# Optimization experiments

Measured on AMD Instinct MI355X. Metric: run time of the kernel, lower is better.

Reference implementation:

```python
import jax, jax.numpy as jnp
import numpy as np

H = 512; EMB = 300; TAGE = 20; TRE = 20
VOCAB = 50000; NTAGS = 50; NTRANS = 100; NCONST = 80
B = 128; S = 256; T = 512; R = S // 2


def _lstm_scan(x, Wih, Whh, b):
    # x: [N, L, D] -> hidden states [N, L, H]; torch gate order i, f, g, o
    N = x.shape[0]; Hh = Whh.shape[1]
    xg = jnp.einsum('nld,gd->nlg', x, Wih) + b  # precompute input projections
    def step(carry, xg_t):
        h, c = carry
        g = xg_t + h @ Whh.T
        i, f, gg, o = jnp.split(g, 4, axis=-1)
        c = jax.nn.sigmoid(f) * c + jax.nn.sigmoid(i) * jnp.tanh(gg)
        h = jax.nn.sigmoid(o) * jnp.tanh(c)
        return (h, c), h
    h0 = jnp.zeros((N, Hh), x.dtype)
    _, hs = jax.lax.scan(step, (h0, h0), jnp.swapaxes(xg, 0, 1))
    return jnp.swapaxes(hs, 0, 1)


def setup_inputs() -> dict:
    key = jax.random.key(0)
    ks = iter(jax.random.split(key, 40))
    def p(shape, scale):
        return jax.random.normal(next(ks), shape, jnp.float32) * jnp.float32(scale)
    def lstm_p(din):
        s = 1.0 / np.sqrt(H)
        return p((4 * H, din), s), p((4 * H, H), s), p((4 * H,), s)
    inp = {}
    inp['word_idx'] = jax.random.randint(next(ks), (B, S), 0, VOCAB)
    inp['tag_idx'] = jax.random.randint(next(ks), (B, S), 0, NTAGS)
    inp['transition_idx'] = jax.random.randint(next(ks), (B, T), 0, NTRANS)
    inp['label_idx'] = jax.random.randint(next(ks), (B, R), 0, NCONST)
    inp['emb'] = p((VOCAB, EMB), 1.0)
    inp['tag_emb'] = p((NTAGS, TAGE), 1.0)
    inp['tr_emb'] = p((NTRANS, TRE), 1.0)
    inp['const_emb'] = p((NCONST, H), 1.0)
    inp['word_Wih'], inp['word_Whh'], inp['word_b'] = lstm_p(EMB + TAGE)
    inp['tr_Wih'], inp['tr_Whh'], inp['tr_b'] = lstm_p(TRE)
    inp['con_Wih'], inp['con_Whh'], inp['con_b'] = lstm_p(H)
    inp['fwd_Wih'], inp['fwd_Whh'], inp['fwd_b'] = lstm_p(H)
    inp['bwd_Wih'], inp['bwd_Whh'], inp['bwd_b'] = lstm_p(H)
    inp['w2c_W'] = p((H, H), 1.0 / np.sqrt(H)); inp['w2c_b'] = jnp.zeros((H,), jnp.float32)
    inp['red_W'] = p((H, 2 * H), 1.0 / np.sqrt(2 * H)); inp['red_b'] = jnp.zeros((H,), jnp.float32)
    inp['out_W'] = p((NTRANS, 3 * H), 1.0 / np.sqrt(3 * H)); inp['out_b'] = jnp.zeros((NTRANS,), jnp.float32)
    return inp


def reference(word_idx, tag_idx, transition_idx, label_idx, emb, tag_emb, tr_emb, const_emb, word_Wih, word_Whh, word_b, tr_Wih, tr_Whh, tr_b, con_Wih, con_Whh, con_b, fwd_Wih, fwd_Whh, fwd_b, bwd_Wih, bwd_Whh, bwd_b, w2c_W, w2c_b, red_W, red_b, out_W, out_b):
    Bn, Sn = word_idx.shape
    Rn = label_idx.shape[1]
    # initial_word_queue: word emb + tag emb -> word LSTM
    word_in = jnp.concatenate([emb[word_idx], tag_emb[tag_idx]], axis=-1)  # [B,S,EMB+TAGE]
    word_h = _lstm_scan(word_in, word_Wih, word_Whh, word_b)              # [B,S,H]
    # transform_word_to_constituent
    c0 = word_h @ w2c_W.T + w2c_b                                         # [B,S,H]
    # build_constituent: label emb + 2 children through fwd/bwd reduce LSTMs
    lab = const_emb[label_idx]                                            # [B,R,H]
    ch0 = c0[:, 0::2][:, :Rn]; ch1 = c0[:, 1::2][:, :Rn]
    fwd_seq = jnp.stack([lab, ch0, ch1], axis=2).reshape(Bn * Rn, 3, -1)
    bwd_seq = jnp.stack([lab, ch1, ch0], axis=2).reshape(Bn * Rn, 3, -1)
    fh = _lstm_scan(fwd_seq, fwd_Wih, fwd_Whh, fwd_b)[:, -1]
    bh = _lstm_scan(bwd_seq, bwd_Wih, bwd_Whh, bwd_b)[:, -1]
    red = jnp.tanh(jnp.concatenate([fh, bh], -1) @ red_W.T + red_b).reshape(Bn, Rn, -1)
    # push_constituent: constituent LSTMCell scan over built constituents
    const_h = _lstm_scan(red, con_Wih, con_Whh, con_b)[:, -1]             # [B,H]
    # push_transition: transition LSTMCell scan
    tr_h = _lstm_scan(tr_emb[transition_idx], tr_Wih, tr_Whh, tr_b)[:, -1]  # [B,H]
    # forward(): W over concat(word_hx, transition_hx, constituent_hx)
    hx = jnp.concatenate([word_h[:, -1], tr_h, const_h], axis=-1)         # [B,3H]
    return hx @ out_W.T + out_b                                           # [B,NTRANS]
```

## Files before the change

### kernel.cpp

```cpp
#include <hip/hip_runtime.h>

typedef unsigned short u16;
typedef unsigned int u32;
typedef unsigned long long u64;
typedef __attribute__((ext_vector_type(8))) short short8;
typedef __attribute__((ext_vector_type(4))) float f32x4;
typedef __attribute__((ext_vector_type(4))) unsigned int u32x4;

namespace {
constexpr int kS  = 256;
constexpr int kT  = 512;
constexpr int kNT = 100;
constexpr int LDST = 40;
constexpr u32 POISON = 0xFFFFFFFFu;
}

__device__ __forceinline__ float bf(u16 v){ return __uint_as_float(((u32)v)<<16); }
__device__ __forceinline__ u16 f2bf(float f){
  u32 u = __float_as_uint(f);
  return (u16)((u + 0x7fffu + ((u>>16)&1u)) >> 16);
}
__device__ __forceinline__ float sigm(float x){ return 1.f/(1.f+__expf(-x)); }
__device__ __forceinline__ float tanha(float x){ return 2.f/(1.f+__expf(-2.f*x)) - 1.f; }
__device__ __forceinline__ float wred(float v){
  #pragma unroll
  for (int off=32; off>0; off>>=1) v += __shfl_xor(v, off, 64);
  return v;
}
__device__ __forceinline__ short8 as_s8(u32x4 x){ union{u32x4 q; short8 v;} u; u.q=x; return u.v; }
__device__ __forceinline__ u32 chk4(u32x4 v){
  return (u32)((v.x==POISON)|(v.y==POISON)|(v.z==POISON)|(v.w==POISON));
}

#define LDX(d, b, o) asm volatile("global_load_dwordx4 %0, %1, off offset:" o : "=v"(d) : "v"(b))
#define LDP(d, b, o) asm volatile("global_load_dwordx4 %0, %1, off offset:" o " sc0 sc1" : "=v"(d) : "v"(b))
#define LDI(d, b)    asm volatile("global_load_dword %0, %1, off" : "=v"(d) : "v"(b))
#define STW(p, v)    asm volatile("global_store_dword %0, %1, off sc0 sc1" :: "v"(p), "v"(v) : "memory")
#define WAITV0       do{ asm volatile("s_waitcnt vmcnt(0)" ::: "memory"); __builtin_amdgcn_sched_barrier(0); }while(0)

__global__ void k_fill(u32* __restrict__ p, int n4){
  const int i = blockIdx.x*256 + threadIdx.x;
  if (i < n4) {
    u32x4 v = {POISON, POISON, POISON, POISON};
    *(u32x4*)&p[(size_t)i*4] = v;
  }
}

struct SeqJob {
  u16* hseq;
  const u16* xg; const int* idx;
  float* c_io;
  const u16* Bw;
  int s_begin, s_end, mode, smask, c_store;
};

__global__ __launch_bounds__(256,1) void k_seq2(SeqJob jA, SeqJob jB)
{
  __shared__ u16 Bs[32*520];
  __shared__ float c_lds[128*9];
  __shared__ float sc[4*4*16*20];
  const SeqJob j = (blockIdx.x < 64) ? jA : jB;
  const int gb = blockIdx.x & 63;
  const int tid = threadIdx.x;
  const int ln = tid & 63, w = tid >> 6, wm = w * 32;
  const int fr = ln & 15, koff = (ln >> 4) * 8;
  const int n0 = gb * 32, jh0 = gb * 8;

  for (int e = tid; e < 2048; e += 256) {
    const int cl_ = e >> 6, kb = (e & 63) * 8;
    *(u32x4*)&Bs[cl_*520 + kb] = *(const u32x4*)&j.Bw[(size_t)(n0+cl_)*512 + kb];
  }
  for (int e = tid; e < 1024; e += 256) {
    const int m = e >> 3, jj = e & 7;
    c_lds[m*9 + jj] = j.c_io[(size_t)m*512 + jh0 + jj];
  }
  __syncthreads();

  const size_t aoff0 = (size_t)(wm + fr)*512 + koff;
  const size_t aoff1 = (size_t)(wm + 16 + fr)*512 + koff;
  const int cr = (ln>>4)*4, cc = ln&15;
  const int trow = ln>>2, pp = ln&3, ntp = pp>>1, cp = pp&1;
  const f32x4 z4 = {0.f,0.f,0.f,0.f};
  const int mA = wm + trow;
  const int mB = wm + 16 + trow;
  const int xgcol = n0 + ntp*16 + cp*8;

  u32x4 xqA, xqB;
  {
    long ivA = mA, ivB = mB;
    if (j.mode == 1) {
      ivA = j.idx[(size_t)mA*512 + j.s_begin];
      ivB = j.idx[(size_t)mB*512 + j.s_begin];
    } else if (j.mode == 2) {
      ivA = (long)mA*128 + j.s_begin;
      ivB = (long)mB*128 + j.s_begin;
    }
    const u16* xgs0 = (j.mode == 0) ? (j.xg + (size_t)j.s_begin*262144) : j.xg;
    const u16* pA = &xgs0[(size_t)ivA*2048 + xgcol];
    const u16* pB = &xgs0[(size_t)ivB*2048 + xgcol];
    LDX(xqA, pA, "0");
    LDX(xqB, pB, "0");
  }
  int inA = 0, inB = 0;

#define PISS(kt, o) LDP(aq0[kt], pa0, o); LDP(aq1[kt], pa1, o)
#define ISSUE_ALL \
  PISS(0,"0");    PISS(1,"64");   PISS(2,"128");  PISS(3,"192"); \
  PISS(4,"256");  PISS(5,"320");  PISS(6,"384");  PISS(7,"448"); \
  PISS(8,"512");  PISS(9,"576");  PISS(10,"640"); PISS(11,"704"); \
  PISS(12,"768"); PISS(13,"832"); PISS(14,"896"); PISS(15,"960")
#define CHECK_ALL(bad) \
  { bad = 0; _Pragma("unroll") \
    for (int kt = 0; kt < 16; ++kt) bad |= chk4(aq0[kt]) | chk4(aq1[kt]); }

  for (int s = j.s_begin; s < j.s_end; ++s) {
    const u16* Ab = j.hseq + (size_t)((s-1) & j.smask)*65536;
    u16* hout     = j.hseq + (size_t)(s & j.smask)*65536;
    const u16* pa0 = Ab + aoff0;
    const u16* pa1 = Ab + aoff1;
    const bool more = (s + 1 < j.s_end);

    if (j.mode == 1 && more) {
      const int* ia = &j.idx[(size_t)mA*512 + s + 1];
      const int* ib = &j.idx[(size_t)mB*512 + s + 1];
      LDI(inA, ia);
      LDI(inB, ib);
    }

    u32x4 aq0[16], aq1[16];
    ISSUE_ALL;
    WAITV0;
    u32 bad; CHECK_ALL(bad);
    while (bad) {
      __builtin_amdgcn_s_sleep(1);
      ISSUE_ALL;
      WAITV0;
      CHECK_ALL(bad);
    }

    f32x4 acc[2][2] = {{z4,z4},{z4,z4}};
    #pragma unroll
    for (int kt = 0; kt < 16; ++kt) {
      const short8 b0 = *(const short8*)&Bs[fr*520 + kt*32 + koff];
      const short8 b1 = *(const short8*)&Bs[(16+fr)*520 + kt*32 + koff];
      const short8 a0v = as_s8(aq0[kt]);
      const short8 a1v = as_s8(aq1[kt]);
      acc[0][0] = __builtin_amdgcn_mfma_f32_16x16x32_bf16(a0v, b0, acc[0][0], 0,0,0);
      acc[0][1] = __builtin_amdgcn_mfma_f32_16x16x32_bf16(a0v, b1, acc[0][1], 0,0,0);
      acc[1][0] = __builtin_amdgcn_mfma_f32_16x16x32_bf16(a1v, b0, acc[1][0], 0,0,0);
      acc[1][1] = __builtin_amdgcn_mfma_f32_16x16x32_bf16(a1v, b1, acc[1][1], 0,0,0);
    }

    #pragma unroll
    for (int mt=0; mt<2; ++mt)
      #pragma unroll
      for (int nt=0; nt<2; ++nt) {
        float* scb = &sc[(size_t)(w*4 + mt*2 + nt)*320];
        #pragma unroll
        for (int ri=0; ri<4; ++ri) scb[(cr+ri)*20 + cc] = acc[mt][nt][ri];
      }
    #pragma unroll
    for (int mt=0; mt<2; ++mt) {
      const int m = mt ? mB : mA;
      const float* scb = &sc[(size_t)(w*4+mt*2+ntp)*320 + trow*20 + cp*8];
      const float4 zlo = *(const float4*)&scb[0];
      const float4 zhi = *(const float4*)&scb[4];
      union { u32x4 u4; u16 h[8]; } xq;
      xq.u4 = mt ? xqB : xqA;
      const int cj = m*9 + ntp*4 + cp*2;
      float h0, h1;
      {
        const float i_ = sigm(zlo.x + bf(xq.h[0]));
        const float f_ = sigm(zlo.y + bf(xq.h[1]));
        const float g_ = tanha(zlo.z + bf(xq.h[2]));
        const float o_ = sigm(zlo.w + bf(xq.h[3]));
        const float cn = f_*c_lds[cj] + i_*g_;
        c_lds[cj] = cn;
        h0 = o_*tanha(cn);
      }
      {
        const float i_ = sigm(zhi.x + bf(xq.h[4]));
        const float f_ = sigm(zhi.y + bf(xq.h[5]));
        const float g_ = tanha(zhi.z + bf(xq.h[6]));
        const float o_ = sigm(zhi.w + bf(xq.h[7]));
        const float cn = f_*c_lds[cj+1] + i_*g_;
        c_lds[cj+1] = cn;
        h1 = o_*tanha(cn);
      }
      const u32 pk = (u32)f2bf(h0) | ((u32)f2bf(h1) << 16);
      u32* hp = (u32*)&hout[(size_t)m*512 + jh0 + ntp*4 + cp*2];
      STW(hp, pk);
    }

    if (more) {
      const u16* xgs1 = (j.mode == 0) ? (j.xg + (size_t)(s+1)*262144) : j.xg;
      long xrA = (j.mode == 0) ? (long)mA : (j.mode == 1 ? (long)inA : ((long)mA*128 + s + 1));
      long xrB = (j.mode == 0) ? (long)mB : (j.mode == 1 ? (long)inB : ((long)mB*128 + s + 1));
      const u16* pA = &xgs1[(size_t)xrA*2048 + xgcol];
      const u16* pB = &xgs1[(size_t)xrB*2048 + xgcol];
      LDX(xqA, pA, "0");
      LDX(xqB, pB, "0");
    }
  }
  if (j.c_store) {
    __syncthreads();
    for (int e = tid; e < 1024; e += 256) {
      const int m = e >> 3, jj = e & 7;
      j.c_io[(size_t)m*512 + jh0 + jj] = c_lds[m*9 + jj];
    }
  }
#undef PISS
#undef ISSUE_ALL
#undef CHECK_ALL
}

__device__ __forceinline__ void gemm_core(
    const u16* __restrict__ A, const u16* __restrict__ B, int K,
    int m0, int n0, u16* As, u16* Bs, f32x4 acc[4][4], int tid)
{
  const int lane = tid & 63;
  const int w = tid >> 6;
  const int wm = (w & 1) * 64, wn = (w >> 1) * 64;
  const int fr = lane & 15;
  const int fq = (lane >> 4) * 8;
  for (int k0 = 0; k0 < K; k0 += 32) {
    __syncthreads();
    #pragma unroll
    for (int it = 0; it < 2; ++it) {
      const int l = tid + it * 256;
      const int r = l >> 2, kq = (l & 3) * 8;
      *(uint4*)&As[r * LDST + kq] = *(const uint4*)&A[(size_t)(m0 + r) * K + k0 + kq];
      *(uint4*)&Bs[r * LDST + kq] = *(const uint4*)&B[(size_t)(n0 + r) * K + k0 + kq];
    }
    __syncthreads();
    short8 af[4], bfr[4];
    #pragma unroll
    for (int t = 0; t < 4; ++t) {
      af[t]  = *(const short8*)&As[(wm + t * 16 + fr) * LDST + fq];
      bfr[t] = *(const short8*)&Bs[(wn + t * 16 + fr) * LDST + fq];
    }
    #pragma unroll
    for (int mt = 0; mt < 4; ++mt)
      #pragma unroll
      for (int nt = 0; nt < 4; ++nt)
        acc[mt][nt] = __builtin_amdgcn_mfma_f32_16x16x32_bf16(af[mt], bfr[nt], acc[mt][nt], 0, 0, 0);
  }
}

__global__ __launch_bounds__(256) void k_gemm(
    const u16* __restrict__ A, const u16* __restrict__ B, u16* __restrict__ C,
    const float* __restrict__ bias, int K, int N, int tanh_flag)
{
  __shared__ u16 As[128 * LDST];
  __shared__ u16 Bs[128 * LDST];
  const int tid = threadIdx.x;
  const int m0 = blockIdx.x * 128, n0 = blockIdx.y * 128;
  f32x4 acc[4][4];
  const f32x4 z4 = {0.f, 0.f, 0.f, 0.f};
  #pragma unroll
  for (int mt = 0; mt < 4; ++mt)
    #pragma unroll
    for (int nt = 0; nt < 4; ++nt) acc[mt][nt] = z4;

  gemm_core(A, B, K, m0, n0, As, Bs, acc, tid);

  const int lane = tid & 63;
  const int w = tid >> 6;
  const int wm = (w & 1) * 64, wn = (w >> 1) * 64;
  const int cr = (lane >> 4) * 4, cc = lane & 15;
  #pragma unroll
  for (int mt = 0; mt < 4; ++mt)
    #pragma unroll
    for (int nt = 0; nt < 4; ++nt)
      #pragma unroll
      for (int ri = 0; ri < 4; ++ri) {
        const int row = m0 + wm + mt * 16 + cr + ri;
        const int col = n0 + wn + nt * 16 + cc;
        float v = acc[mt][nt][ri];
        if (bias) v += bias[col];
        if (tanh_flag) v = tanha(v);
        C[(size_t)row * N + col] = f2bf(v);
      }
}

__global__ __launch_bounds__(256) void k_lstm_cat(
    const u16* __restrict__ H, const u16* __restrict__ X,
    const u16* __restrict__ B, const float* __restrict__ bias,
    const int* __restrict__ idx, int cmode, int p0, int first,
    float* __restrict__ c_st, u16* __restrict__ h_out, int h_stride, int h_coloff)
{
  __shared__ u16 As[128 * LDST];
  __shared__ u16 Bs[128 * LDST];
  __shared__ float zb[64 * 128];
  const int tid = threadIdx.x;
  const int m0 = blockIdx.x * 128, n0 = blockIdx.y * 128;
  const int lane = tid & 63;
  const int w = tid >> 6;
  const int wm = (w & 1) * 64, wn = (w >> 1) * 64;
  const int fr = lane & 15, fq = (lane >> 4) * 8;
  f32x4 acc[4][4];
  const f32x4 z4 = {0.f, 0.f, 0.f, 0.f};
  #pragma unroll
  for (int mt = 0; mt < 4; ++mt)
    #pragma unroll
    for (int nt = 0; nt < 4; ++nt) acc[mt][nt] = z4;

  for (int k0 = first ? 512 : 0; k0 < 1024; k0 += 32) {
    __syncthreads();
    #pragma unroll
    for (int it = 0; it < 2; ++it) {
      const int l = tid + it * 256;
      const int r = l >> 2, kq = (l & 3) * 8;
      const int m = m0 + r;
      const u16* src;
      if (k0 < 512) {
        src = H + (size_t)m * 512 + k0 + kq;
      } else {
        long xr;
        if (cmode == 1)      xr = (long)(2 * (m & 127) + p0) * 128 + (m >> 7);
        else if (cmode == 2) xr = (long)idx[m];
        else                 xr = (long)m * 128 + p0;
        src = X + (size_t)xr * 512 + (k0 - 512) + kq;
      }
      *(uint4*)&As[r * LDST + kq] = *(const uint4*)src;
      *(uint4*)&Bs[r * LDST + kq] = *(const uint4*)&B[(size_t)(n0 + r) * 1024 + k0 + kq];
    }
    __syncthreads();
    short8 af[4], bfr[4];
    #pragma unroll
    for (int t = 0; t < 4; ++t) {
      af[t]  = *(const short8*)&As[(wm + t * 16 + fr) * LDST + fq];
      bfr[t] = *(const short8*)&Bs[(wn + t * 16 + fr) * LDST + fq];
    }
    #pragma unroll
    for (int mt = 0; mt < 4; ++mt)
      #pragma unroll
      for (int nt = 0; nt < 4; ++nt)
        acc[mt][nt] = __builtin_amdgcn_mfma_f32_16x16x32_bf16(af[mt], bfr[nt], acc[mt][nt], 0, 0, 0);
  }

  const int cr = (lane >> 4) * 4, cc = lane & 15;
  #pragma unroll
  for (int half = 0; half < 2; ++half) {
    __syncthreads();
    if (wm == half * 64) {
      #pragma unroll
      for (int mt = 0; mt < 4; ++mt)
        #pragma unroll
        for (int nt = 0; nt < 4; ++nt)
          #pragma unroll
          for (int ri = 0; ri < 4; ++ri)
            zb[(mt * 16 + cr + ri) * 128 + wn + nt * 16 + cc] = acc[mt][nt][ri];
    }
    __syncthreads();
    for (int c = tid; c < 2048; c += 256) {
      const int rl = c >> 5;
      const int q  = c & 31;
      const int m  = m0 + half * 64 + rl;
      const int jh = (n0 >> 2) + q;
      const float4 bv = *(const float4*)&bias[n0 + q * 4];
      const float4 zv = *(const float4*)&zb[rl * 128 + q * 4];
      const float i_ = sigm(zv.x + bv.x);
      const float f_ = sigm(zv.y + bv.y);
      const float g_ = tanha(zv.z + bv.z);
      const float o_ = sigm(zv.w + bv.w);
      const size_t ci = (size_t)m * 512 + jh;
      const float cold = first ? 0.f : c_st[ci];
      const float cn = f_ * cold + i_ * g_;
      c_st[ci] = cn;
      h_out[(size_t)m * h_stride + h_coloff + jh] = f2bf(o_ * tanha(cn));
    }
  }
}

__global__ __launch_bounds__(256) void k_gate0(
    const u16* __restrict__ xg, int xg_mode, int p0,
    const int* __restrict__ idx, int istride,
    float* __restrict__ c_st, u16* __restrict__ h_out, int h_stride, int h_coloff, int M)
{
  const int id = blockIdx.x * 256 + threadIdx.x;
  if (id >= M * 512) return;
  const int m = id >> 9, jh = id & 511;
  long xr;
  if (xg_mode == 0) xr = (long)m * p0;
  else              xr = (long)idx[(size_t)m * istride];
  const ushort4 xq = *(const ushort4*)&xg[(size_t)xr * 2048 + jh * 4];
  const float i_ = sigm(bf(xq.x));
  const float g_ = tanha(bf(xq.z));
  const float o_ = sigm(bf(xq.w));
  const float cn = i_ * g_;
  c_st[(size_t)m * 512 + jh] = cn;
  h_out[(size_t)m * h_stride + h_coloff + jh] = f2bf(o_ * tanha(cn));
}

__global__ void k_perm_w(const float* __restrict__ in, u16* __restrict__ out,
                         int Ksrc, int Kfill, int Ktot, int coff)
{
  const int rp = blockIdx.x;
  const int g = rp & 3, jh = rp >> 2;
  const float* src = in + (size_t)(g * 512 + jh) * Ksrc;
  for (int k = threadIdx.x; k < Kfill; k += 256)
    out[(size_t)rp * Ktot + coff + k] = f2bf(k < Ksrc ? src[k] : 0.f);
}
__global__ void k_perm_b(const float* __restrict__ in, float* __restrict__ out)
{
  const int rp = blockIdx.x * 256 + threadIdx.x;
  out[rp] = in[(rp & 3) * 512 + (rp >> 2)];
}
__global__ void k_cvt(const float* __restrict__ in, u16* __restrict__ out, int n)
{
  const int i = blockIdx.x * 256 + threadIdx.x;
  if (i < n) out[i] = f2bf(in[i]);
}
__global__ void k_pad2d(const float* __restrict__ in, u16* __restrict__ out,
                        int Rin, int Kin, int Kout)
{
  const int r = blockIdx.x;
  for (int k = threadIdx.x; k < Kout; k += 256)
    out[(size_t)r * Kout + k] = f2bf((r < Rin && k < Kin) ? in[(size_t)r * Kin + k] : 0.f);
}
__global__ void k_gather_word(const int* __restrict__ widx, const int* __restrict__ tidx,
                              const float* __restrict__ emb, const float* __restrict__ temb,
                              u16* __restrict__ Aw)
{
  const int row = blockIdx.x;
  const int s = row >> 7, b = row & 127;
  const int wi = widx[b * kS + s];
  const int ti = tidx[b * kS + s];
  for (int t = threadIdx.x; t < 320; t += 256)
    Aw[(size_t)row * 320 + t] = f2bf(t < 300 ? emb[(size_t)wi * 300 + t] : temb[ti * 20 + t - 300]);
}

__global__ __launch_bounds__(256) void k_out(
    const u16* __restrict__ wh, const u16* __restrict__ trh, const u16* __restrict__ conh,
    const float* __restrict__ W, const float* __restrict__ bias, float* __restrict__ out)
{
  const int wid = blockIdx.x * 4 + (threadIdx.x >> 6);
  const int lane = threadIdx.x & 63;
  const int b = wid / kNT;
  const int t = wid - b * kNT;
  const u16* s0 = wh + (size_t)b * 512;
  const u16* s1 = trh + (size_t)b * 512;
  const u16* s2 = conh + (size_t)b * 512;
  const float* wr = W + (size_t)t * 1536;
  float acc = 0.f;
  #pragma unroll
  for (int i = 0; i < 8; ++i) acc += bf(s0[i * 64 + lane]) * wr[i * 64 + lane];
  #pragma unroll
  for (int i = 0; i < 8; ++i) acc += bf(s1[i * 64 + lane]) * wr[512 + i * 64 + lane];
  #pragma unroll
  for (int i = 0; i < 8; ++i) acc += bf(s2[i * 64 + lane]) * wr[1024 + i * 64 + lane];
  acc = wred(acc);
  if (lane == 0) out[(size_t)b * kNT + t] = acc + bias[t];
}

extern "C" void kernel_launch(void* const* d_in, const int* in_sizes, int n_in,
                              void* d_out, int out_size, void* d_ws, size_t ws_size,
                              hipStream_t stream)
{
  (void)in_sizes; (void)n_in; (void)out_size; (void)ws_size;
  const int* word_idx = (const int*)d_in[0];
  const int* tag_idx  = (const int*)d_in[1];
  const int* tr_idx   = (const int*)d_in[2];
  const int* lab_idx  = (const int*)d_in[3];
  const float* emb       = (const float*)d_in[4];
  const float* tag_emb   = (const float*)d_in[5];
  const float* tr_emb    = (const float*)d_in[6];
  const float* const_emb = (const float*)d_in[7];
  const float* word_Wih = (const float*)d_in[8];
  const float* word_Whh = (const float*)d_in[9];
  const float* word_b   = (const float*)d_in[10];
  const float* tr_Wih = (const float*)d_in[11];
  const float* tr_Whh = (const float*)d_in[12];
  const float* tr_b   = (const float*)d_in[13];
  const float* con_Wih = (const float*)d_in[14];
  const float* con_Whh = (const float*)d_in[15];
  const float* con_b   = (const float*)d_in[16];
  const float* fwd_Wih = (const float*)d_in[17];
  const float* fwd_Whh = (const float*)d_in[18];
  const float* fwd_b   = (const float*)d_in[19];
  const float* bwd_Wih = (const float*)d_in[20];
  const float* bwd_Whh = (const float*)d_in[21];
  const float* bwd_b   = (const float*)d_in[22];
  const float* w2c_W = (const float*)d_in[23];
  const float* w2c_b = (const float*)d_in[24];
  const float* red_W = (const float*)d_in[25];
  const float* red_b = (const float*)d_in[26];
  const float* out_W = (const float*)d_in[27];
  const float* out_b = (const float*)d_in[28];

  char* p = (char*)d_ws;
  auto alloc = [&](size_t bytes)->void* {
    void* r = (void*)p; p += (bytes + 255) & ~(size_t)255; return r;
  };
  u16* word_h = (u16*)alloc((size_t)33554432);
  char* R     = (char*)alloc((size_t)167772160);
  u16* A_word = (u16*)(R);
  u16* XGword = (u16*)(R + 33554432);
  u16* trseq  = (u16*)(R);
  u16* c0     = (u16*)(R + 33554432);
  u16* h1     = (u16*)(R + 67108864);
  u16* h2     = (u16*)(R + 83886080);
  float* c_big= (float*)(R + 100663296);
  u16* fb     = (u16*)(R + 134217728);
  u16* red    = (u16*)(R);
  u16* XG_con = (u16*)(R + 67108864);
  u16* conseq = (u16*)(R + 134217728);
  u16* wWih = (u16*)alloc((size_t)2048*320*2);
  u16* wWhh = (u16*)alloc((size_t)2048*512*2);
  u16* tWih = (u16*)alloc((size_t)2048*32*2);
  u16* tWhh = (u16*)alloc((size_t)2048*512*2);
  u16* cWihp = (u16*)alloc((size_t)2048*512*2);
  u16* cWhhp = (u16*)alloc((size_t)2048*512*2);
  u16* fWcat = (u16*)alloc((size_t)2048*1024*2);
  u16* bWcat = (u16*)alloc((size_t)2048*1024*2);
  u16* fWih  = (u16*)alloc((size_t)2048*512*2);
  u16* bWih  = (u16*)alloc((size_t)2048*512*2);
  u16* w2cWb = (u16*)alloc((size_t)512*512*2);
  u16* redWb = (u16*)alloc((size_t)512*1024*2);
  u16* A80   = (u16*)alloc((size_t)128*512*2);
  u16* Atr   = (u16*)alloc((size_t)128*32*2);
  u16* tbltr = (u16*)alloc((size_t)128*2048*2);
  u16* tbl0  = (u16*)alloc((size_t)128*2048*2);
  float* b_word = (float*)alloc(2048*4);
  float* b_tr   = (float*)alloc(2048*4);
  float* b_con  = (float*)alloc(2048*4);
  float* b_fwd  = (float*)alloc(2048*4);
  float* b_bwd  = (float*)alloc(2048*4);
  float* c_word = (float*)alloc((size_t)128*512*4);
  float* c_tr   = (float*)alloc((size_t)128*512*4);
  float* c_con  = (float*)alloc((size_t)128*512*4);

  k_perm_w<<<2048,256,0,stream>>>(word_Wih, wWih, 320, 320, 320, 0);
  k_perm_w<<<2048,256,0,stream>>>(word_Whh, wWhh, 512, 512, 512, 0);
  k_perm_w<<<2048,256,0,stream>>>(tr_Wih,   tWih, 20,  32,  32,  0);
  k_perm_w<<<2048,256,0,stream>>>(tr_Whh,   tWhh, 512, 512, 512, 0);
  k_perm_w<<<2048,256,0,stream>>>(con_Wih,  cWihp, 512, 512, 512, 0);
  k_perm_w<<<2048,256,0,stream>>>(con_Whh,  cWhhp, 512, 512, 512, 0);
  k_perm_w<<<2048,256,0,stream>>>(fwd_Whh,  fWcat, 512, 512, 1024, 0);
  k_perm_w<<<2048,256,0,stream>>>(fwd_Wih,  fWcat, 512, 512, 1024, 512);
  k_perm_w<<<2048,256,0,stream>>>(bwd_Whh,  bWcat, 512, 512, 1024, 0);
  k_perm_w<<<2048,256,0,stream>>>(bwd_Wih,  bWcat, 512, 512, 1024, 512);
  k_perm_w<<<2048,256,0,stream>>>(fwd_Wih,  fWih, 512, 512, 512, 0);
  k_perm_w<<<2048,256,0,stream>>>(bwd_Wih,  bWih, 512, 512, 512, 0);
  k_perm_b<<<8,256,0,stream>>>(word_b, b_word);
  k_perm_b<<<8,256,0,stream>>>(tr_b,   b_tr);
  k_perm_b<<<8,256,0,stream>>>(con_b,  b_con);
  k_perm_b<<<8,256,0,stream>>>(fwd_b,  b_fwd);
  k_perm_b<<<8,256,0,stream>>>(bwd_b,  b_bwd);
  k_cvt<<<1024,256,0,stream>>>(w2c_W, w2cWb, 512*512);
  k_cvt<<<2048,256,0,stream>>>(red_W, redWb, 512*1024);
  k_pad2d<<<128,256,0,stream>>>(const_emb, A80, 80, 512, 512);
  k_pad2d<<<128,256,0,stream>>>(tr_emb,    Atr, 100, 20, 32);
  k_gather_word<<<32768,256,0,stream>>>(word_idx, tag_idx, emb, tag_emb, A_word);

  k_gemm<<<dim3(256,16),256,0,stream>>>(A_word, wWih, XGword, b_word, 320, 2048, 0);
  k_gemm<<<dim3(1,16),256,0,stream>>>(Atr, tWih, tbltr, b_tr, 32, 2048, 0);

  k_fill<<<8160,256,0,stream>>>((u32*)(word_h + 65536), 2088960);
  k_fill<<<8160,256,0,stream>>>((u32*)(trseq + 65536), 2088960);

  k_gate0<<<256,256,0,stream>>>(XGword, 0, 1, nullptr, 0, c_word, word_h, 512, 0, 128);
  k_gate0<<<256,256,0,stream>>>(tbltr, 2, 0, tr_idx, 512, c_tr, trseq, 512, 0, 128);

  SeqJob jw { word_h, XGword, nullptr, c_word, wWhh, 1, 256, 0, 255, 0 };
  SeqJob jt1{ trseq,  tbltr,  tr_idx,  c_tr,   tWhh, 1, 256, 1, 511, 1 };
  k_seq2<<<128,256,0,stream>>>(jw, jt1);

  k_gemm<<<dim3(256,4),256,0,stream>>>(word_h, w2cWb, c0, w2c_b, 512, 512, 0);

  k_gemm<<<dim3(1,16),256,0,stream>>>(A80, fWih, tbl0, b_fwd, 512, 2048, 0);
  k_gate0<<<32768,256,0,stream>>>(tbl0, 2, 0, lab_idx, 1, c_big, h1, 512, 0, 16384);
  k_lstm_cat<<<dim3(128,16),256,0,stream>>>(h1, c0, fWcat, b_fwd, nullptr, 1, 0, 0, c_big, h2, 512, 0);
  k_lstm_cat<<<dim3(128,16),256,0,stream>>>(h2, c0, fWcat, b_fwd, nullptr, 1, 1, 0, c_big, fb, 1024, 0);
  k_gemm<<<dim3(1,16),256,0,stream>>>(A80, bWih, tbl0, b_bwd, 512, 2048, 0);
  k_gate0<<<32768,256,0,stream>>>(tbl0, 2, 0, lab_idx, 1, c_big, h1, 512, 0, 16384);
  k_lstm_cat<<<dim3(128,16),256,0,stream>>>(h1, c0, bWcat, b_bwd, nullptr, 1, 1, 0, c_big, h2, 512, 0);
  k_lstm_cat<<<dim3(128,16),256,0,stream>>>(h2, c0, bWcat, b_bwd, nullptr, 1, 0, 0, c_big, fb, 1024, 512);

  k_gemm<<<dim3(128,4),256,0,stream>>>(fb, redWb, red, red_b, 1024, 512, 1);

  k_gemm<<<dim3(128,16),256,0,stream>>>(red, cWihp, XG_con, b_con, 512, 2048, 0);

  k_fill<<<8192,256,0,stream>>>((u32*)(trseq + (size_t)256*65536), 2097152);
  k_fill<<<4064,256,0,stream>>>((u32*)(conseq + 65536), 1040384);

  k_gate0<<<256,256,0,stream>>>(XG_con, 0, 128, nullptr, 0, c_con, conseq, 512, 0, 128);

  SeqJob jc { conseq, XG_con, nullptr, c_con, cWhhp, 1,   128, 2, 255, 0 };
  SeqJob jt2{ trseq,  tbltr,  tr_idx,  c_tr,  tWhh,  256, 512, 1, 511, 0 };
  k_seq2<<<128,256,0,stream>>>(jc, jt2);

  k_out<<<3200,256,0,stream>>>(word_h + (size_t)255*65536, trseq + (size_t)511*65536,
                               conseq + (size_t)127*65536, out_W, out_b, (float*)d_out);
}
```

Measured before the change: 6.373 ms.

## Replace poison-polling recurrence sync with per-step flags and XCD-local block placement

The persistent LSTM recurrence kernel stops spinning on poison-filled hidden-state buffers and instead uses per-block step flags, published after a block barrier and polled by one wavefront. The kernel now launches 512 blocks and discovers which blocks share an XCD by probing L2 visibility. When one group of 64 co-located blocks is verified, it runs a job using L2-scoped (sc0) loads and stores instead of system-coherent ones. This also removes the poison fill kernels. The cost is a complex startup handshake and extra idle blocks, with a fallback to the old placement and system-scope traffic if discovery fails. It also relies on undocumented XCD scheduling behaviour.

```diff
diff --git a/kernel.cpp b/kernel.cpp
--- a/kernel.cpp
+++ b/kernel.cpp
@@ -12,7 +12,6 @@
 constexpr int kT  = 512;
 constexpr int kNT = 100;
 constexpr int LDST = 40;
-constexpr u32 POISON = 0xFFFFFFFFu;
 }
 
 __device__ __forceinline__ float bf(u16 v){ return __uint_as_float(((u32)v)<<16); }
@@ -28,22 +27,41 @@
   return v;
 }
 __device__ __forceinline__ short8 as_s8(u32x4 x){ union{u32x4 q; short8 v;} u; u.q=x; return u.v; }
-__device__ __forceinline__ u32 chk4(u32x4 v){
-  return (u32)((v.x==POISON)|(v.y==POISON)|(v.z==POISON)|(v.w==POISON));
-}
-
-#define LDX(d, b, o) asm volatile("global_load_dwordx4 %0, %1, off offset:" o : "=v"(d) : "v"(b))
-#define LDP(d, b, o) asm volatile("global_load_dwordx4 %0, %1, off offset:" o " sc0 sc1" : "=v"(d) : "v"(b))
-#define LDI(d, b)    asm volatile("global_load_dword %0, %1, off" : "=v"(d) : "v"(b))
-#define STW(p, v)    asm volatile("global_store_dword %0, %1, off sc0 sc1" :: "v"(p), "v"(v) : "memory")
-#define WAITV0       do{ asm volatile("s_waitcnt vmcnt(0)" ::: "memory"); __builtin_amdgcn_sched_barrier(0); }while(0)
-
-__global__ void k_fill(u32* __restrict__ p, int n4){
+
+__device__ __forceinline__ void st_sys_u32(u32* p, u32 v){
+  __hip_atomic_store(p, v, __ATOMIC_RELAXED, __HIP_MEMORY_SCOPE_SYSTEM);
+}
+__device__ __forceinline__ u32 ld_sys_u32(const u32* p){
+  return __hip_atomic_load(p, __ATOMIC_RELAXED, __HIP_MEMORY_SCOPE_SYSTEM);
+}
+
+#define WAITV0 do{ asm volatile("s_waitcnt vmcnt(0)" ::: "memory"); __builtin_amdgcn_sched_barrier(0); }while(0)
+
+template<bool L> __device__ __forceinline__ void ldh(u32x4& d, const u16* p){
+  if constexpr (L) asm volatile("global_load_dwordx4 %0, %1, off sc0" : "=v"(d) : "v"(p));
+  else             asm volatile("global_load_dwordx4 %0, %1, off"     : "=v"(d) : "v"(p));
+}
+__device__ __forceinline__ void ldi(int& d, const int* p){
+  asm volatile("global_load_dword %0, %1, off" : "=v"(d) : "v"(p));
+}
+template<bool L> __device__ __forceinline__ void st_h(u32* p, u32 v){
+  if constexpr (L) asm volatile("global_store_dword %0, %1, off sc0"     :: "v"(p), "v"(v) : "memory");
+  else             asm volatile("global_store_dword %0, %1, off sc0 sc1" :: "v"(p), "v"(v) : "memory");
+}
+template<bool L> __device__ __forceinline__ u32 ld_flag(const u32* p){
+  u32 f;
+  if constexpr (L) asm volatile("global_load_dword %0, %1, off sc0\n\ts_waitcnt vmcnt(0)"     : "=v"(f) : "v"(p) : "memory");
+  else             asm volatile("global_load_dword %0, %1, off sc0 sc1\n\ts_waitcnt vmcnt(0)" : "=v"(f) : "v"(p) : "memory");
+  __builtin_amdgcn_sched_barrier(0);
+  return f;
+}
+__device__ __forceinline__ void st_l2_u32(u32* p, u32 v){
+  asm volatile("global_store_dword %0, %1, off sc0" :: "v"(p), "v"(v) : "memory");
+}
+
+__global__ void k_zero(u32* p, int n){
   const int i = blockIdx.x*256 + threadIdx.x;
-  if (i < n4) {
-    u32x4 v = {POISON, POISON, POISON, POISON};
-    *(u32x4*)&p[(size_t)i*4] = v;
-  }
+  if (i < n) p[i] = 0;
 }
 
 struct SeqJob {
@@ -51,17 +69,14 @@
   const u16* xg; const int* idx;
   float* c_io;
   const u16* Bw;
+  u32* flags;
   int s_begin, s_end, mode, smask, c_store;
 };
 
-__global__ __launch_bounds__(256,1) void k_seq2(SeqJob jA, SeqJob jB)
-{
-  __shared__ u16 Bs[32*520];
-  __shared__ float c_lds[128*9];
-  __shared__ float sc[4*4*16*20];
-  const SeqJob j = (blockIdx.x < 64) ? jA : jB;
-  const int gb = blockIdx.x & 63;
-  const int tid = threadIdx.x;
+template<bool LOCAL>
+__device__ void seq_loop(const SeqJob j, const int gb, const int tid,
+                         u16* Bs, float* c_lds, float* sc)
+{
   const int ln = tid & 63, w = tid >> 6, wm = w * 32;
   const int fr = ln & 15, koff = (ln >> 4) * 8;
   const int n0 = gb * 32, jh0 = gb * 8;
@@ -96,22 +111,10 @@
       ivB = (long)mB*128 + j.s_begin;
     }
     const u16* xgs0 = (j.mode == 0) ? (j.xg + (size_t)j.s_begin*262144) : j.xg;
-    const u16* pA = &xgs0[(size_t)ivA*2048 + xgcol];
-    const u16* pB = &xgs0[(size_t)ivB*2048 + xgcol];
-    LDX(xqA, pA, "0");
-    LDX(xqB, pB, "0");
+    ldh<false>(xqA, &xgs0[(size_t)ivA*2048 + xgcol]);
+    ldh<false>(xqB, &xgs0[(size_t)ivB*2048 + xgcol]);
   }
   int inA = 0, inB = 0;
-
-#define PISS(kt, o) LDP(aq0[kt], pa0, o); LDP(aq1[kt], pa1, o)
-#define ISSUE_ALL \
-  PISS(0,"0");    PISS(1,"64");   PISS(2,"128");  PISS(3,"192"); \
-  PISS(4,"256");  PISS(5,"320");  PISS(6,"384");  PISS(7,"448"); \
-  PISS(8,"512");  PISS(9,"576");  PISS(10,"640"); PISS(11,"704"); \
-  PISS(12,"768"); PISS(13,"832"); PISS(14,"896"); PISS(15,"960")
-#define CHECK_ALL(bad) \
-  { bad = 0; _Pragma("unroll") \
-    for (int kt = 0; kt < 16; ++kt) bad |= chk4(aq0[kt]) | chk4(aq1[kt]); }
 
   for (int s = j.s_begin; s < j.s_end; ++s) {
     const u16* Ab = j.hseq + (size_t)((s-1) & j.smask)*65536;
@@ -121,22 +124,17 @@
     const bool more = (s + 1 < j.s_end);
 
     if (j.mode == 1 && more) {
-      const int* ia = &j.idx[(size_t)mA*512 + s + 1];
-      const int* ib = &j.idx[(size_t)mB*512 + s + 1];
-      LDI(inA, ia);
-      LDI(inB, ib);
+      ldi(inA, &j.idx[(size_t)mA*512 + s + 1]);
+      ldi(inB, &j.idx[(size_t)mB*512 + s + 1]);
     }
 
     u32x4 aq0[16], aq1[16];
-    ISSUE_ALL;
+    #pragma unroll
+    for (int kt = 0; kt < 16; ++kt) {
+      ldh<LOCAL>(aq0[kt], pa0 + kt*32);
+      ldh<LOCAL>(aq1[kt], pa1 + kt*32);
+    }
     WAITV0;
-    u32 bad; CHECK_ALL(bad);
-    while (bad) {
-      __builtin_amdgcn_s_sleep(1);
-      ISSUE_ALL;
-      WAITV0;
-      CHECK_ALL(bad);
-    }
 
     f32x4 acc[2][2] = {{z4,z4},{z4,z4}};
     #pragma unroll
@@ -188,18 +186,27 @@
         h1 = o_*tanha(cn);
       }
       const u32 pk = (u32)f2bf(h0) | ((u32)f2bf(h1) << 16);
-      u32* hp = (u32*)&hout[(size_t)m*512 + jh0 + ntp*4 + cp*2];
-      STW(hp, pk);
-    }
-
+      st_h<LOCAL>((u32*)&hout[(size_t)m*512 + jh0 + ntp*4 + cp*2], pk);
+    }
+
+    __builtin_amdgcn_s_waitcnt(0);
+    __syncthreads();
+    if (tid == 0) st_h<LOCAL>(&j.flags[gb], (u32)s);
     if (more) {
       const u16* xgs1 = (j.mode == 0) ? (j.xg + (size_t)(s+1)*262144) : j.xg;
       long xrA = (j.mode == 0) ? (long)mA : (j.mode == 1 ? (long)inA : ((long)mA*128 + s + 1));
       long xrB = (j.mode == 0) ? (long)mB : (j.mode == 1 ? (long)inB : ((long)mB*128 + s + 1));
-      const u16* pA = &xgs1[(size_t)xrA*2048 + xgcol];
-      const u16* pB = &xgs1[(size_t)xrB*2048 + xgcol];
-      LDX(xqA, pA, "0");
-      LDX(xqB, pB, "0");
+      ldh<false>(xqA, &xgs1[(size_t)xrA*2048 + xgcol]);
+      ldh<false>(xqB, &xgs1[(size_t)xrB*2048 + xgcol]);
+      if (tid < 64) {
+        const u32* fp = j.flags + tid;
+        while (true) {
+          u32 f = ld_flag<LOCAL>(fp);
+          if (__all((int)(f >= (u32)s))) break;
+          __builtin_amdgcn_s_sleep(1);
+        }
+      }
+      __syncthreads();
     }
   }
   if (j.c_store) {
@@ -209,9 +216,113 @@
       j.c_io[(size_t)m*512 + jh0 + jj] = c_lds[m*9 + jj];
     }
   }
-#undef PISS
-#undef ISSUE_ALL
-#undef CHECK_ALL
+}
+
+__global__ __launch_bounds__(256,1) void k_seq2(SeqJob jA, SeqJob jB, u32* d)
+{
+  __shared__ u16 Bs[32*520];
+  __shared__ float c_lds[128*9];
+  __shared__ float sc[4*4*16*20];
+  __shared__ u64 bmc[8], bmp[8];
+  __shared__ int s_state, s_rank, s_leader, s_job, s_abort;
+  __shared__ u32 s_hash;
+  const int tid = threadIdx.x;
+  const int bid = blockIdx.x;
+  u32* tok = d;
+  u32* hsh = d + 512;
+  u32* jsl = d + 1024;
+  u32* msc = d + 1536;
+
+  if (tid == 0) {
+    st_l2_u32(&tok[bid], 1u);
+    #pragma unroll
+    for (int i = 0; i < 8; ++i) bmp[i] = ~0ull;
+    s_state = 0;
+  }
+  __syncthreads();
+  {
+    int stc = 0;
+    for (int it = 0; it < 1200; ++it) {
+      const u32 t0 = ld_flag<true>(&tok[tid]);
+      const u32 t1 = ld_flag<true>(&tok[256 + tid]);
+      const u64 b0 = __ballot(t0 != 0u);
+      const u64 b1 = __ballot(t1 != 0u);
+      if ((tid & 63) == 0) { bmc[tid>>6] = b0; bmc[4+(tid>>6)] = b1; }
+      __syncthreads();
+      if (tid == 0) {
+        bool same = true; int pc = 0;
+        for (int i = 0; i < 8; ++i) {
+          same = same && (bmc[i] == bmp[i]);
+          bmp[i] = bmc[i];
+          pc += __popcll(bmc[i]);
+        }
+        stc = same ? stc + 1 : 0;
+        if (stc >= 3) s_state = (pc == 64) ? 1 : 2;
+      }
+      __syncthreads();
+      if (s_state != 0) break;
+      __builtin_amdgcn_s_sleep(2);
+    }
+  }
+
+  int verified = 0;
+  if (s_state == 1) {
+    if (tid == 0) {
+      u32 h = 0x9E3779B9u;
+      for (int i = 0; i < 8; ++i) {
+        h ^= (u32)bmp[i] * 2654435761u + (u32)(bmp[i]>>32) * 40503u + (u32)i;
+        h = (h << 13) | (h >> 19);
+      }
+      h |= 0x80000000u;
+      s_hash = h;
+      int r = 0, ld = -1;
+      for (int i = 0; i < 8; ++i) {
+        const u64 m = bmp[i];
+        if (ld < 0 && m) ld = i*64 + (__ffsll((unsigned long long)m) - 1);
+        if (i < (bid >> 6)) r += __popcll(m);
+        else if (i == (bid >> 6)) r += __popcll(m & ((1ull << (bid & 63)) - 1ull));
+      }
+      s_rank = r; s_leader = ld;
+      st_l2_u32(&hsh[bid], h);
+    }
+    __syncthreads();
+    for (int it = 0; it < 1200; ++it) {
+      const u32 mh = s_hash;
+      const int bit0 = (int)((bmp[tid>>6] >> (tid & 63)) & 1ull);
+      const int bit1 = (int)((bmp[4+(tid>>6)] >> (tid & 63)) & 1ull);
+      const int ok0 = !bit0 || (ld_flag<true>(&hsh[tid]) == mh);
+      const int ok1 = !bit1 || (ld_flag<true>(&hsh[256 + tid]) == mh);
+      if (__syncthreads_and(ok0 && ok1)) { verified = 1; break; }
+      __builtin_amdgcn_s_sleep(2);
+    }
+  }
+
+  if (tid == 0) {
+    if (!verified) st_sys_u32(&msc[0], 1u);
+    __builtin_amdgcn_s_waitcnt(0);
+    __hip_atomic_fetch_add(&msc[1], 1u, __ATOMIC_RELAXED, __HIP_MEMORY_SCOPE_SYSTEM);
+    while (ld_sys_u32(&msc[1]) < 512u) __builtin_amdgcn_s_sleep(8);
+    s_abort = (int)ld_sys_u32(&msc[0]);
+  }
+  __syncthreads();
+
+  if (!s_abort) {
+    if (tid == 0) {
+      if (s_rank == 0) {
+        const u32 jv = __hip_atomic_fetch_add(&msc[2], 1u, __ATOMIC_RELAXED, __HIP_MEMORY_SCOPE_SYSTEM);
+        st_l2_u32(&jsl[bid], jv + 1u);
+      }
+      u32 v;
+      do { v = ld_flag<true>(&jsl[s_leader]); if (!v) __builtin_amdgcn_s_sleep(2); } while (!v);
+      s_job = (int)v - 1;
+    }
+    __syncthreads();
+    if (s_job >= 2) return;
+    seq_loop<true>(s_job ? jB : jA, s_rank, tid, Bs, c_lds, sc);
+  } else {
+    if (bid < 64)       seq_loop<false>(jA, bid, tid, Bs, c_lds, sc);
+    else if (bid < 128) seq_loop<false>(jB, bid - 64, tid, Bs, c_lds, sc);
+  }
 }
 
 __device__ __forceinline__ void gemm_core(
@@ -530,6 +641,10 @@
   float* c_word = (float*)alloc((size_t)128*512*4);
   float* c_tr   = (float*)alloc((size_t)128*512*4);
   float* c_con  = (float*)alloc((size_t)128*512*4);
+  u32* flags = (u32*)alloc((size_t)4*64*4);
+  u32* dsc   = (u32*)alloc((size_t)2*2048*4);
+
+  k_zero<<<17,256,0,stream>>>(flags, 256 + 4096);
 
   k_perm_w<<<2048,256,0,stream>>>(word_Wih, wWih, 320, 320, 320, 0);
   k_perm_w<<<2048,256,0,stream>>>(word_Whh, wWhh, 512, 512, 512, 0);
@@ -557,15 +672,12 @@
   k_gemm<<<dim3(256,16),256,0,stream>>>(A_word, wWih, XGword, b_word, 320, 2048, 0);
   k_gemm<<<dim3(1,16),256,0,stream>>>(Atr, tWih, tbltr, b_tr, 32, 2048, 0);
 
-  k_fill<<<8160,256,0,stream>>>((u32*)(word_h + 65536), 2088960);
-  k_fill<<<8160,256,0,stream>>>((u32*)(trseq + 65536), 2088960);
-
   k_gate0<<<256,256,0,stream>>>(XGword, 0, 1, nullptr, 0, c_word, word_h, 512, 0, 128);
   k_gate0<<<256,256,0,stream>>>(tbltr, 2, 0, tr_idx, 512, c_tr, trseq, 512, 0, 128);
 
-  SeqJob jw { word_h, XGword, nullptr, c_word, wWhh, 1, 256, 0, 255, 0 };
-  SeqJob jt1{ trseq,  tbltr,  tr_idx,  c_tr,   tWhh, 1, 256, 1, 511, 1 };
-  k_seq2<<<128,256,0,stream>>>(jw, jt1);
+  SeqJob jw { word_h, XGword, nullptr, c_word, wWhh, flags + 0*64, 1, 256, 0, 255, 0 };
+  SeqJob jt1{ trseq,  tbltr,  tr_idx,  c_tr,   tWhh, flags + 1*64, 1, 256, 1, 511, 1 };
+  k_seq2<<<512,256,0,stream>>>(jw, jt1, dsc);
 
   k_gemm<<<dim3(256,4),256,0,stream>>>(word_h, w2cWb, c0, w2c_b, 512, 512, 0);
 
@@ -582,14 +694,11 @@
 
   k_gemm<<<dim3(128,16),256,0,stream>>>(red, cWihp, XG_con, b_con, 512, 2048, 0);
 
-  k_fill<<<8192,256,0,stream>>>((u32*)(trseq + (size_t)256*65536), 2097152);
-  k_fill<<<4064,256,0,stream>>>((u32*)(conseq + 65536), 1040384);
-
   k_gate0<<<256,256,0,stream>>>(XG_con, 0, 128, nullptr, 0, c_con, conseq, 512, 0, 128);
 
-  SeqJob jc { conseq, XG_con, nullptr, c_con, cWhhp, 1,   128, 2, 255, 0 };
-  SeqJob jt2{ trseq,  tbltr,  tr_idx,  c_tr,  tWhh,  256, 512, 1, 511, 0 };
-  k_seq2<<<128,256,0,stream>>>(jc, jt2);
+  SeqJob jc { conseq, XG_con, nullptr, c_con, cWhhp, flags + 2*64, 1,   128, 2, 255, 0 };
+  SeqJob jt2{ trseq,  tbltr,  tr_idx,  c_tr,  tWhh,  flags + 3*64, 256, 512, 1, 511, 0 };
+  k_seq2<<<512,256,0,stream>>>(jc, jt2, dsc + 2048);
 
   k_out<<<3200,256,0,stream>>>(word_h + (size_t)255*65536, trseq + (size_t)511*65536,
                                conseq + (size_t)127*65536, out_W, out_b, (float*)d_out);
```

New measurement: 6.342 ms. About the same (-0.5%).

## Replace poison-polling handoff with per-wave step flags in recurrent kernel

Applied to the files above, without the earlier changes.

The persistent recurrent kernel used to fill the hidden-state buffers with a poison value and spin-reload all A operands until none were poisoned. It now has each wave publish a step counter flag after its hidden-state stores drain, and consumers poll 256 flags before loading the previous step once. This drops the large poison-fill kernels and the repeated full-operand reloads. In exchange it adds a flag poll with serial uncached loads and a vmcnt wait per step, and correctness now depends on store-then-flag ordering.

```diff
diff --git a/kernel.cpp b/kernel.cpp
--- a/kernel.cpp
+++ b/kernel.cpp
@@ -12,7 +12,6 @@
 constexpr int kT  = 512;
 constexpr int kNT = 100;
 constexpr int LDST = 40;
-constexpr u32 POISON = 0xFFFFFFFFu;
 }
 
 __device__ __forceinline__ float bf(u16 v){ return __uint_as_float(((u32)v)<<16); }
@@ -28,22 +27,28 @@
   return v;
 }
 __device__ __forceinline__ short8 as_s8(u32x4 x){ union{u32x4 q; short8 v;} u; u.q=x; return u.v; }
-__device__ __forceinline__ u32 chk4(u32x4 v){
-  return (u32)((v.x==POISON)|(v.y==POISON)|(v.z==POISON)|(v.w==POISON));
-}
-
-#define LDX(d, b, o) asm volatile("global_load_dwordx4 %0, %1, off offset:" o : "=v"(d) : "v"(b))
-#define LDP(d, b, o) asm volatile("global_load_dwordx4 %0, %1, off offset:" o " sc0 sc1" : "=v"(d) : "v"(b))
-#define LDI(d, b)    asm volatile("global_load_dword %0, %1, off" : "=v"(d) : "v"(b))
-#define STW(p, v)    asm volatile("global_store_dword %0, %1, off sc0 sc1" :: "v"(p), "v"(v) : "memory")
-#define WAITV0       do{ asm volatile("s_waitcnt vmcnt(0)" ::: "memory"); __builtin_amdgcn_sched_barrier(0); }while(0)
-
-__global__ void k_fill(u32* __restrict__ p, int n4){
+
+#define WAITV0 do{ asm volatile("s_waitcnt vmcnt(0)" ::: "memory"); __builtin_amdgcn_sched_barrier(0); }while(0)
+
+__device__ __forceinline__ void ldc(u32x4& d, const u16* p){
+  asm volatile("global_load_dwordx4 %0, %1, off" : "=v"(d) : "v"(p));
+}
+__device__ __forceinline__ void ldi(int& d, const int* p){
+  asm volatile("global_load_dword %0, %1, off" : "=v"(d) : "v"(p));
+}
+__device__ __forceinline__ void stw(u32* p, u32 v){
+  asm volatile("global_store_dword %0, %1, off sc0 sc1" :: "v"(p), "v"(v) : "memory");
+}
+__device__ __forceinline__ u32 ldf(const u32* p){
+  u32 f;
+  asm volatile("global_load_dword %0, %1, off sc0 sc1\n\ts_waitcnt vmcnt(0)" : "=v"(f) : "v"(p) : "memory");
+  __builtin_amdgcn_sched_barrier(0);
+  return f;
+}
+
+__global__ void k_zero(u32* p, int n){
   const int i = blockIdx.x*256 + threadIdx.x;
-  if (i < n4) {
-    u32x4 v = {POISON, POISON, POISON, POISON};
-    *(u32x4*)&p[(size_t)i*4] = v;
-  }
+  if (i < n) p[i] = 0;
 }
 
 struct SeqJob {
@@ -51,6 +56,7 @@
   const u16* xg; const int* idx;
   float* c_io;
   const u16* Bw;
+  u32* flags;
   int s_begin, s_end, mode, smask, c_store;
 };
 
@@ -84,6 +90,7 @@
   const int mA = wm + trow;
   const int mB = wm + 16 + trow;
   const int xgcol = n0 + ntp*16 + cp*8;
+  u32* const myflag = j.flags + gb*4 + w;
 
   u32x4 xqA, xqB;
   {
@@ -96,22 +103,10 @@
       ivB = (long)mB*128 + j.s_begin;
     }
     const u16* xgs0 = (j.mode == 0) ? (j.xg + (size_t)j.s_begin*262144) : j.xg;
-    const u16* pA = &xgs0[(size_t)ivA*2048 + xgcol];
-    const u16* pB = &xgs0[(size_t)ivB*2048 + xgcol];
-    LDX(xqA, pA, "0");
-    LDX(xqB, pB, "0");
+    ldc(xqA, &xgs0[(size_t)ivA*2048 + xgcol]);
+    ldc(xqB, &xgs0[(size_t)ivB*2048 + xgcol]);
   }
   int inA = 0, inB = 0;
-
-#define PISS(kt, o) LDP(aq0[kt], pa0, o); LDP(aq1[kt], pa1, o)
-#define ISSUE_ALL \
-  PISS(0,"0");    PISS(1,"64");   PISS(2,"128");  PISS(3,"192"); \
-  PISS(4,"256");  PISS(5,"320");  PISS(6,"384");  PISS(7,"448"); \
-  PISS(8,"512");  PISS(9,"576");  PISS(10,"640"); PISS(11,"704"); \
-  PISS(12,"768"); PISS(13,"832"); PISS(14,"896"); PISS(15,"960")
-#define CHECK_ALL(bad) \
-  { bad = 0; _Pragma("unroll") \
-    for (int kt = 0; kt < 16; ++kt) bad |= chk4(aq0[kt]) | chk4(aq1[kt]); }
 
   for (int s = j.s_begin; s < j.s_end; ++s) {
     const u16* Ab = j.hseq + (size_t)((s-1) & j.smask)*65536;
@@ -120,23 +115,32 @@
     const u16* pa1 = Ab + aoff1;
     const bool more = (s + 1 < j.s_end);
 
+    if (s > j.s_begin) {
+      const u32 tgt = (u32)(s - 1);
+      const u32* f0 = j.flags + ln;
+      while (true) {
+        const u32 a = ldf(f0);
+        const u32 b = ldf(f0 + 64);
+        const u32 c = ldf(f0 + 128);
+        const u32 d = ldf(f0 + 192);
+        const int ok = (a >= tgt) & (b >= tgt) & (c >= tgt) & (d >= tgt);
+        if (__all(ok)) break;
+        __builtin_amdgcn_s_sleep(1);
+      }
+    }
+
     if (j.mode == 1 && more) {
-      const int* ia = &j.idx[(size_t)mA*512 + s + 1];
-      const int* ib = &j.idx[(size_t)mB*512 + s + 1];
-      LDI(inA, ia);
-      LDI(inB, ib);
+      ldi(inA, &j.idx[(size_t)mA*512 + s + 1]);
+      ldi(inB, &j.idx[(size_t)mB*512 + s + 1]);
     }
 
     u32x4 aq0[16], aq1[16];
-    ISSUE_ALL;
+    #pragma unroll
+    for (int kt = 0; kt < 16; ++kt) {
+      ldc(aq0[kt], pa0 + kt*32);
+      ldc(aq1[kt], pa1 + kt*32);
+    }
     WAITV0;
-    u32 bad; CHECK_ALL(bad);
-    while (bad) {
-      __builtin_amdgcn_s_sleep(1);
-      ISSUE_ALL;
-      WAITV0;
-      CHECK_ALL(bad);
-    }
 
     f32x4 acc[2][2] = {{z4,z4},{z4,z4}};
     #pragma unroll
@@ -188,18 +192,17 @@
         h1 = o_*tanha(cn);
       }
       const u32 pk = (u32)f2bf(h0) | ((u32)f2bf(h1) << 16);
-      u32* hp = (u32*)&hout[(size_t)m*512 + jh0 + ntp*4 + cp*2];
-      STW(hp, pk);
-    }
-
+      stw((u32*)&hout[(size_t)m*512 + jh0 + ntp*4 + cp*2], pk);
+    }
+
+    WAITV0;
+    if (ln == 0) stw(myflag, (u32)s);
     if (more) {
       const u16* xgs1 = (j.mode == 0) ? (j.xg + (size_t)(s+1)*262144) : j.xg;
       long xrA = (j.mode == 0) ? (long)mA : (j.mode == 1 ? (long)inA : ((long)mA*128 + s + 1));
       long xrB = (j.mode == 0) ? (long)mB : (j.mode == 1 ? (long)inB : ((long)mB*128 + s + 1));
-      const u16* pA = &xgs1[(size_t)xrA*2048 + xgcol];
-      const u16* pB = &xgs1[(size_t)xrB*2048 + xgcol];
-      LDX(xqA, pA, "0");
-      LDX(xqB, pB, "0");
+      ldc(xqA, &xgs1[(size_t)xrA*2048 + xgcol]);
+      ldc(xqB, &xgs1[(size_t)xrB*2048 + xgcol]);
     }
   }
   if (j.c_store) {
@@ -209,9 +212,6 @@
       j.c_io[(size_t)m*512 + jh0 + jj] = c_lds[m*9 + jj];
     }
   }
-#undef PISS
-#undef ISSUE_ALL
-#undef CHECK_ALL
 }
 
 __device__ __forceinline__ void gemm_core(
@@ -530,6 +530,9 @@
   float* c_word = (float*)alloc((size_t)128*512*4);
   float* c_tr   = (float*)alloc((size_t)128*512*4);
   float* c_con  = (float*)alloc((size_t)128*512*4);
+  u32* flags = (u32*)alloc((size_t)4*256*4);
+
+  k_zero<<<4,256,0,stream>>>(flags, 4*256);
 
   k_perm_w<<<2048,256,0,stream>>>(word_Wih, wWih, 320, 320, 320, 0);
   k_perm_w<<<2048,256,0,stream>>>(word_Whh, wWhh, 512, 512, 512, 0);
@@ -557,14 +560,11 @@
   k_gemm<<<dim3(256,16),256,0,stream>>>(A_word, wWih, XGword, b_word, 320, 2048, 0);
   k_gemm<<<dim3(1,16),256,0,stream>>>(Atr, tWih, tbltr, b_tr, 32, 2048, 0);
 
-  k_fill<<<8160,256,0,stream>>>((u32*)(word_h + 65536), 2088960);
-  k_fill<<<8160,256,0,stream>>>((u32*)(trseq + 65536), 2088960);
-
   k_gate0<<<256,256,0,stream>>>(XGword, 0, 1, nullptr, 0, c_word, word_h, 512, 0, 128);
   k_gate0<<<256,256,0,stream>>>(tbltr, 2, 0, tr_idx, 512, c_tr, trseq, 512, 0, 128);
 
-  SeqJob jw { word_h, XGword, nullptr, c_word, wWhh, 1, 256, 0, 255, 0 };
-  SeqJob jt1{ trseq,  tbltr,  tr_idx,  c_tr,   tWhh, 1, 256, 1, 511, 1 };
+  SeqJob jw { word_h, XGword, nullptr, c_word, wWhh, flags + 0*256, 1, 256, 0, 255, 0 };
+  SeqJob jt1{ trseq,  tbltr,  tr_idx,  c_tr,   tWhh, flags + 1*256, 1, 256, 1, 511, 1 };
   k_seq2<<<128,256,0,stream>>>(jw, jt1);
 
   k_gemm<<<dim3(256,4),256,0,stream>>>(word_h, w2cWb, c0, w2c_b, 512, 512, 0);
@@ -582,13 +582,10 @@
 
   k_gemm<<<dim3(128,16),256,0,stream>>>(red, cWihp, XG_con, b_con, 512, 2048, 0);
 
-  k_fill<<<8192,256,0,stream>>>((u32*)(trseq + (size_t)256*65536), 2097152);
-  k_fill<<<4064,256,0,stream>>>((u32*)(conseq + 65536), 1040384);
-
   k_gate0<<<256,256,0,stream>>>(XG_con, 0, 128, nullptr, 0, c_con, conseq, 512, 0, 128);
 
-  SeqJob jc { conseq, XG_con, nullptr, c_con, cWhhp, 1,   128, 2, 255, 0 };
-  SeqJob jt2{ trseq,  tbltr,  tr_idx,  c_tr,  tWhh,  256, 512, 1, 511, 0 };
+  SeqJob jc { conseq, XG_con, nullptr, c_con, cWhhp, flags + 2*256, 1,   128, 2, 255, 0 };
+  SeqJob jt2{ trseq,  tbltr,  tr_idx,  c_tr,  tWhh,  flags + 3*256, 256, 512, 1, 511, 0 };
   k_seq2<<<128,256,0,stream>>>(jc, jt2);
 
   k_out<<<3200,256,0,stream>>>(word_h + (size_t)255*65536, trseq + (size_t)511*65536,
```

After: 5.742 ms. -9.9%, faster.
